# Performance work log

Hardware: AMD Instinct MI355X
Metric: run time of the kernel (lower is better)

The kernel has to match this reference:

```python
import jax, jax.numpy as jnp
import numpy as np

B, D, H = 256, 512, 256
K = 5
MARGIN = 1.0
TAU = 1.0
LAM_C = 0.01
LAM_E = 0.1
BETA = 0.1
LN_EPS = 1e-5


def _layernorm(x, g, b):
    mu = jnp.mean(x, axis=-1, keepdims=True)
    var = jnp.var(x, axis=-1, keepdims=True)
    return (x - mu) * jax.lax.rsqrt(var + LN_EPS) * g + b


def setup_inputs() -> dict:
    key = jax.random.key(0)
    ks = jax.random.split(key, 16)
    s = 0.02
    inp = {
        "outputs": jax.random.normal(ks[0], (B, 3, 64, 64), jnp.float32),
        "images": jax.random.normal(ks[1], (B, 3, 64, 64), jnp.float32),
        "f_orig": jax.random.normal(ks[2], (B, D), jnp.float32),
        "f_recon": jax.random.normal(ks[3], (B, D), jnp.float32),
        "cf1": jax.random.normal(ks[4], (B, 256, 8, 8), jnp.float32),
        "cf2": jax.random.normal(ks[5], (B, 512, 4, 4), jnp.float32),
        # EnergyNet encoder params
        "W1": jax.random.normal(ks[6], (D, H), jnp.float32) * s,
        "b1": jnp.zeros((H,), jnp.float32),
        "g1": jnp.ones((H,), jnp.float32),
        "be1": jnp.zeros((H,), jnp.float32),
        "W2": jax.random.normal(ks[7], (H, H), jnp.float32) * s,
        "b2": jnp.zeros((H,), jnp.float32),
        # EnergyNet interaction params
        "W3": jax.random.normal(ks[8], (3 * H, H), jnp.float32) * s,
        "b3": jnp.zeros((H,), jnp.float32),
        "g3": jnp.ones((H,), jnp.float32),
        "be3": jnp.zeros((H,), jnp.float32),
        "W4": jax.random.normal(ks[9], (H, H // 2), jnp.float32) * s,
        "b4": jnp.zeros((H // 2,), jnp.float32),
        "W5": jax.random.normal(ks[10], (H // 2, 1), jnp.float32) * s,
        "b5": jnp.zeros((1,), jnp.float32),
    }
    return inp


def _encoder(x, W1, b1, g1, be1, W2, b2):
    h = _layernorm(x @ W1 + b1, g1, be1)
    return jax.nn.relu(h) @ W2 + b2


def _energy_matrix(f1, f2, W1, b1, g1, be1, W2, b2, W3, b3, g3, be3, W4, b4, W5, b5):
    e1 = _encoder(f1, W1, b1, g1, be1, W2, b2)  # [B,H]
    e2 = _encoder(f2, W1, b1, g1, be1, W2, b2)  # [B,H]
    e1b = jnp.broadcast_to(e1[:, None, :], (B, B, H))
    e2b = jnp.broadcast_to(e2[None, :, :], (B, B, H))
    combined = jnp.concatenate([e1b, e2b, e1b * e2b], axis=-1)  # [B,B,3H]
    h = jax.nn.relu(_layernorm(combined @ W3 + b3, g3, be3))
    h = jax.nn.relu(h @ W4 + b4)
    return (h @ W5 + b5)[..., 0]  # [B,B]


def _topk_neighbors(f, k):
    fn = f / (jnp.linalg.norm(f, axis=1, keepdims=True))
    sim = fn @ fn.T
    sim = jnp.where(jnp.eye(f.shape[0], dtype=bool), -jnp.inf, sim)
    _, idx = jax.lax.top_k(sim, k)  # [B,k]
    onehot = jnp.zeros((f.shape[0], f.shape[0]), jnp.float32)
    rows = jnp.arange(f.shape[0])[:, None]
    return onehot.at[rows, idx].set(1.0)


def _entropy(x):
    xn = (x - x.min()) / (x.max() - x.min() + 1e-8)
    # torch.histc(bins=256, min=0, max=1): values at max go to last bin
    idx = jnp.clip(jnp.floor(xn.reshape(-1) * 256.0).astype(jnp.int32), 0, 255)
    hist = jnp.bincount(idx, length=256).astype(jnp.float32)
    p = hist / hist.sum()
    return -jnp.sum(p * jnp.log2(p + 1e-8))


def reference(outputs, images, f_orig, f_recon, cf1, cf2,
              W1, b1, g1, be1, W2, b2, W3, b3, g3, be3, W4, b4, W5, b5):
    # reconstruction loss
    recon = jnp.mean((outputs - images) ** 2)

    # energy margin loss
    E = _energy_matrix(f_orig, f_recon, W1, b1, g1, be1, W2, b2,
                       W3, b3, g3, be3, W4, b4, W5, b5)
    pos = jnp.diag(E)[:, None]
    losses = jax.nn.relu(MARGIN + E - pos)
    neg_mask = ~jnp.eye(B, dtype=bool)
    standard_loss = jnp.sum(losses * neg_mask) / (B * (B - 1))

    k = min(K, B - 1)
    on = _topk_neighbors(f_orig, k)
    rn = _topk_neighbors(f_recon, k)
    inter = jnp.sum(on * rn, axis=1)
    union = jnp.sum(jnp.clip(on + rn, 0.0, 1.0), axis=1)
    jaccard = inter / (union + 1e-8)
    neighbor_loss = 1.0 - jnp.mean(jaccard)
    energy_loss = standard_loss + 0.3 * neighbor_loss

    # compression loss over the dict of compressed features {cf1, cf2}
    sp = 0.5 * (jnp.mean(jnp.abs(cf1)) + jnp.mean(jnp.abs(cf2)))
    en = 0.5 * (_entropy(cf1) + _entropy(cf2))
    compress = sp + BETA * en

    total = recon + LAM_C * compress + LAM_E * energy_loss
    return (total, recon, energy_loss, compress)
```

## Files before the change

### kernel.cpp

```cpp
#include <hip/hip_runtime.h>
#include <math.h>

typedef __attribute__((ext_vector_type(8))) short short8;
typedef __attribute__((ext_vector_type(4))) float f32x4;
typedef __attribute__((ext_vector_type(4))) unsigned int u32x4;

union U8 { unsigned int u[4]; short8 s; u32x4 v; };


__device__ __forceinline__ float wave_sum(float v) {
#pragma unroll
    for (int o = 32; o > 0; o >>= 1) v += __shfl_down(v, o);
    return v;
}

__device__ __forceinline__ float block_sum256(float v, float* red) {
    v = wave_sum(v);
    int t = threadIdx.x;
    if ((t & 63) == 0) red[t >> 6] = v;
    __syncthreads();
    float r = red[0] + red[1] + red[2] + red[3];
    __syncthreads();
    return r;
}

__device__ __forceinline__ unsigned fenc(float f) {
    unsigned u = __float_as_uint(f);
    return (u & 0x80000000u) ? ~u : (u | 0x80000000u);
}
__device__ __forceinline__ float fdec(unsigned u) {
    return (u & 0x80000000u) ? __uint_as_float(u & 0x7fffffffu) : __uint_as_float(~u);
}

__device__ __forceinline__ ushort f2bf(float f) {
    unsigned u = __float_as_uint(f);
    unsigned r = (u + 0x7fffu + ((u >> 16) & 1u)) >> 16;
    return (ushort)r;
}
__device__ __forceinline__ float bflo(unsigned u) { return __uint_as_float(u << 16); }
__device__ __forceinline__ float bfhi(unsigned u) { return __uint_as_float(u & 0xffff0000u); }


__global__ void init_kernel(float* wsf, unsigned* wsu, int* wsi) {
    int t = threadIdx.x;
    if (t < 7) wsf[t] = 0.f;
    if (t == 7 || t == 9) wsu[t] = 0xFFFFFFFFu;
    if (t == 8 || t == 10) wsu[t] = 0u;
    wsi[16 + t] = 0;
    wsi[272 + t] = 0;
}

__global__ __launch_bounds__(256) void mega_kernel(
    const float4* __restrict__ o, const float4* __restrict__ im,
    const float4* __restrict__ cf1, const float4* __restrict__ cf2,
    const float* __restrict__ fo, const float* __restrict__ fr,
    const float* __restrict__ W1, const float* __restrict__ b1,
    const float* __restrict__ g1, const float* __restrict__ be1,
    const float* __restrict__ W2, const float* __restrict__ b2,
    const float* __restrict__ W3,
    float* wsf, unsigned* wsu, float* rnorm, float* fT,
    float* __restrict__ A1, ushort* __restrict__ A2bf, ushort* __restrict__ ebf,
    ushort* __restrict__ W3pk, ushort* __restrict__ W4pk, const float* __restrict__ W4) {
    __shared__ float smem[64 * 33];
    float* red = smem;
    int b = blockIdx.x, t = threadIdx.x;
    if (b < 2048) {
        if (b < 512) {
            float s = 0.f;
            for (int i = b * 256 + t; i < 786432; i += 512 * 256) {
                float4 a = o[i], c = im[i];
                float dx = a.x - c.x, dy = a.y - c.y, dz = a.z - c.z, dw = a.w - c.w;
                s += dx * dx + dy * dy + dz * dz + dw * dw;
            }
            float tot = block_sum256(s, red);
            if (t == 0) atomicAdd(wsf + 0, tot);
        } else if (b < 1536) {
            int which = (b < 1024) ? 0 : 1;
            const float4* x = which ? cf2 : cf1;
            int n4 = which ? 524288 : 1048576;
            int b0 = which ? 1024 : 512;
            float s = 0.f, mn = INFINITY, mx = -INFINITY;
            for (int i = (b - b0) * 256 + t; i < n4; i += 512 * 256) {
                float4 a = x[i];
                s += fabsf(a.x) + fabsf(a.y) + fabsf(a.z) + fabsf(a.w);
                mn = fminf(mn, fminf(fminf(a.x, a.y), fminf(a.z, a.w)));
                mx = fmaxf(mx, fmaxf(fmaxf(a.x, a.y), fmaxf(a.z, a.w)));
            }
            float tot = block_sum256(s, red);
#pragma unroll
            for (int off = 32; off > 0; off >>= 1) {
                mn = fminf(mn, __shfl_down(mn, off));
                mx = fmaxf(mx, __shfl_down(mx, off));
            }
            float* rmn = smem + 8;
            float* rmx = smem + 16;
            if ((t & 63) == 0) { rmn[t >> 6] = mn; rmx[t >> 6] = mx; }
            __syncthreads();
            if (t == 0) {
                atomicAdd(wsf + 1 + which, tot);
                float m1 = fminf(fminf(rmn[0], rmn[1]), fminf(rmn[2], rmn[3]));
                float m2 = fmaxf(fmaxf(rmx[0], rmx[1]), fmaxf(rmx[2], rmx[3]));
                atomicMin(wsu + 7 + which * 2, fenc(m1));
                atomicMax(wsu + 8 + which * 2, fenc(m2));
            }
        } else {
            int r = b - 1536;
            const float4* f = (r < 256) ? ((const float4*)fo + (size_t)r * 128)
                                        : ((const float4*)fr + (size_t)(r - 256) * 128);
            float s = 0.f;
            if (t < 128) {
                float4 a = f[t];
                s = a.x * a.x + a.y * a.y + a.z * a.z + a.w * a.w;
            }
            float tot = block_sum256(s, red);
            if (t == 0) rnorm[r] = 1.0f / sqrtf(tot);
        }
    } else if (b < 2176) {
        int bb = b - 2048;
        int pass = bb >> 6;
        int kt = (bb >> 2) & 15;
        int jt = bb & 3;
        int k0 = kt * 32, j0 = jt * 64;
        const float* f = pass ? fr : fo;
        float (*tile)[33] = (float(*)[33])smem;
        int cl = t & 31, rl = t >> 5;
#pragma unroll
        for (int r = 0; r < 8; ++r) {
            int row = j0 + rl + r * 8;
            tile[rl + r * 8][cl] = f[(size_t)row * 512 + k0 + cl];
        }
        __syncthreads();
        int jl = t & 63, kq = t >> 6;
        float* dst = fT + (size_t)pass * 131072;
#pragma unroll
        for (int c = 0; c < 8; ++c) {
            int kl = kq * 8 + c;
            dst[(size_t)(k0 + kl) * 256 + j0 + jl] = tile[jl][kl];
        }
    } else if (b < 2224) {
        int pb = b - 2176;
        const float* W3c = W3 + 512 * 256;
        if (pb < 32) {
            int s = pb * 256 + t;
            int lane = s & 63;
            int tt = (s >> 6) & 15;
            int kk = s >> 10;
            int qq = lane >> 4, nn = lane & 15;
            int tcol = tt * 16 + nn;
            short8 v;
#pragma unroll
            for (int jj = 0; jj < 8; ++jj) {
                int k = kk * 32 + qq * 8 + jj;
                v[jj] = (short)f2bf(W3c[(size_t)k * 256 + tcol]);
            }
            *(short8*)(W3pk + (size_t)s * 8) = v;
        } else {
            int s = (pb - 32) * 256 + t;
            int lane = s & 63;
            int tt = (s >> 6) & 7;
            int kk = s >> 9;
            int qq = lane >> 4, nn = lane & 15;
            int ncol = tt * 16 + nn;
            short8 v;
#pragma unroll
            for (int jj = 0; jj < 8; ++jj) {
                int k = kk * 32 + qq * 8 + jj;
                v[jj] = (short)f2bf(W4[(size_t)k * 128 + ncol]);
            }
            *(short8*)(W4pk + (size_t)s * 8) = v;
        }
    } else {
        int r = b - 2224;
        const float* f = (r < 256) ? (fo + (size_t)r * 512) : (fr + (size_t)(r - 256) * 512);
        const float* W3p = (r < 256) ? W3 : (W3 + 256 * 256);
        float* fs = smem;
        float* hs = smem + 512;
        float* es = smem + 768;
        float* rd = smem + 1024;
        fs[t] = f[t];
        fs[t + 256] = f[t + 256];
        __syncthreads();
        float x = b1[t];
        for (int k = 0; k < 512; ++k) x += fs[k] * W1[k * 256 + t];
        float s1 = block_sum256(x, rd);
        float s2 = block_sum256(x * x, rd);
        float mean = s1 * (1.f / 256.f);
        float var = s2 * (1.f / 256.f) - mean * mean;
        float rstd = rsqrtf(var + 1e-5f);
        float hn = (x - mean) * rstd * g1[t] + be1[t];
        hs[t] = fmaxf(hn, 0.f);
        __syncthreads();
        float e = b2[t];
        for (int k = 0; k < 256; ++k) e += hs[k] * W2[k * 256 + t];
        ebf[(size_t)r * 256 + t] = f2bf(e);
        es[t] = e;
        __syncthreads();
        float a = 0.f;
        for (int k = 0; k < 256; ++k) a += es[k] * W3p[k * 256 + t];
        if (r < 256) A1[(size_t)r * 256 + t] = a;
        else A2bf[(size_t)(r - 256) * 256 + t] = f2bf(a);
    }
}

__global__ __launch_bounds__(256) void hist_kernel(const float4* __restrict__ cf1,
                                                   const float4* __restrict__ cf2,
                                                   const unsigned* wsu, int* wsi) {
    __shared__ int hl[256];
    int b = blockIdx.x, t = threadIdx.x;
    hl[t] = 0;
    __syncthreads();
    int which = (b < 512) ? 0 : 1;
    const float4* x = which ? cf2 : cf1;
    int n4 = which ? 524288 : 1048576;
    int b0 = which ? 512 : 0;
    int* hist = wsi + (which ? 272 : 16);
    float mn = fdec(wsu[7 + which * 2]), mx = fdec(wsu[8 + which * 2]);
    float inv = 256.f / (mx - mn + 1e-8f);
    for (int i = (b - b0) * 256 + t; i < n4; i += 512 * 256) {
        float4 a = x[i];
        int b0i = min(max((int)floorf((a.x - mn) * inv), 0), 255);
        int b1i = min(max((int)floorf((a.y - mn) * inv), 0), 255);
        int b2i = min(max((int)floorf((a.z - mn) * inv), 0), 255);
        int b3i = min(max((int)floorf((a.w - mn) * inv), 0), 255);
        atomicAdd(&hl[b0i], 1);
        atomicAdd(&hl[b1i], 1);
        atomicAdd(&hl[b2i], 1);
        atomicAdd(&hl[b3i], 1);
    }
    __syncthreads();
    if (hl[t]) atomicAdd(&hist[t], hl[t]);
}

__global__ __launch_bounds__(256) void simtop_kernel(const float* __restrict__ fo,
                                                     const float* __restrict__ fr,
                                                     const float* __restrict__ rnorm,
                                                     const float* __restrict__ fT,
                                                     int* __restrict__ top5) {
    int b = blockIdx.x;
    int pass = b >> 7, pair = b & 127;
    int i0 = pair * 2, i1 = i0 + 1;
    const float* f = pass ? fr : fo;
    const float* rn = rnorm + pass * 256;
    __shared__ float2 fs2[512];
    __shared__ float candV[4][2][5];
    __shared__ int candI[4][2][5];
    int t = threadIdx.x;
    const float* f0 = f + (size_t)i0 * 512;
    const float* f1 = f + (size_t)i1 * 512;
    fs2[t] = make_float2(f0[t], f1[t]);
    fs2[t + 256] = make_float2(f0[t + 256], f1[t + 256]);
    __syncthreads();
    int j = t;
    const float* col = fT + (size_t)pass * 131072 + j;
    float a0 = 0.f, a1 = 0.f;
#pragma unroll 16
    for (int k = 0; k < 512; ++k) {
        float v = col[(size_t)k * 256];
        float2 fv = fs2[k];
        a0 += fv.x * v;
        a1 += fv.y * v;
    }
    float rnj = rn[j];
    a0 *= rnj;
    a1 *= rnj;
    if (j == i0) a0 = -INFINITY;
    if (j == i1) a1 = -INFINITY;
    int w = t >> 6, lane = t & 63;
    for (int sel = 0; sel < 2; ++sel) {
        float v2 = sel ? a1 : a0;
        int idx = j;
        for (int r = 0; r < 5; ++r) {
            float m = v2;
            int mi = idx;
#pragma unroll
            for (int off = 32; off > 0; off >>= 1) {
                float om = __shfl_xor(m, off);
                int omi = __shfl_xor(mi, off);
                if (om > m || (om == m && omi < mi)) { m = om; mi = omi; }
            }
            if (lane == 0) { candV[w][sel][r] = m; candI[w][sel][r] = mi; }
            if (idx == mi) v2 = -INFINITY;
        }
    }
    __syncthreads();
    if (w < 2) {
        float v = -INFINITY;
        int ix = 0x7fffffff;
        if (lane < 20) { v = candV[lane / 5][w][lane % 5]; ix = candI[lane / 5][w][lane % 5]; }
        int iSel = w ? i1 : i0;
        for (int r = 0; r < 5; ++r) {
            float m = v;
            int mi = ix;
#pragma unroll
            for (int off = 32; off > 0; off >>= 1) {
                float om = __shfl_xor(m, off);
                int omi = __shfl_xor(mi, off);
                if (om > m || (om == m && omi < mi)) { m = om; mi = omi; }
            }
            if (lane == 0) top5[((size_t)pass * 256 + iSel) * 5 + r] = mi;
            if (ix == mi) v = -INFINITY;
        }
    }
}

__global__ __launch_bounds__(256, 1) void energy_v3(
    const float* __restrict__ A1, const ushort* __restrict__ A2bf,
    const ushort* __restrict__ ebf,
    const ushort* __restrict__ W3p, const ushort* __restrict__ W4p,
    const float* __restrict__ b3, const float* __restrict__ g3, const float* __restrict__ be3,
    const float* __restrict__ b4, const float* __restrict__ W5, const float* __restrict__ b5,
    float* __restrict__ E)
{
    int i = blockIdx.x;
    int t = threadIdx.x;
    int w = t >> 6, lane = t & 63, q = lane >> 4, n = lane & 15;
    int jb = w * 64;
    __shared__ float combS[256], g3S[256], be3S[256], b4S[128], w5S[128];
    combS[t] = A1[(size_t)i * 256 + t] + b3[t];
    g3S[t] = g3[t];
    be3S[t] = be3[t];
    if (t < 128) { b4S[t] = b4[t]; w5S[t] = W5[t]; }
    __syncthreads();

    const ushort* e1p = ebf + (size_t)i * 256;
    const ushort* e2p = ebf + 65536;

    f32x4 acc[4][16];
#pragma unroll
    for (int s = 0; s < 4; ++s)
#pragma unroll
        for (int tt = 0; tt < 16; ++tt) acc[s][tt] = (f32x4){0.f, 0.f, 0.f, 0.f};

    for (int kk = 0; kk < 8; ++kk) {
        int kbase = kk * 32 + q * 8;
        U8 e1v;
        e1v.v = *(const u32x4*)(e1p + kbase);
        float e1f[8];
#pragma unroll
        for (int x = 0; x < 4; ++x) {
            e1f[2 * x] = bflo(e1v.u[x]);
            e1f[2 * x + 1] = bfhi(e1v.u[x]);
        }
        short8 bfrag[4];
#pragma unroll
        for (int s = 0; s < 4; ++s) {
            U8 e2v;
            e2v.v = *(const u32x4*)(e2p + (size_t)(jb + s * 16 + n) * 256 + kbase);
            U8 bb;
#pragma unroll
            for (int x = 0; x < 4; ++x) {
                float p0 = bflo(e2v.u[x]) * e1f[2 * x];
                float p1 = bfhi(e2v.u[x]) * e1f[2 * x + 1];
                bb.u[x] = (unsigned)f2bf(p0) | ((unsigned)f2bf(p1) << 16);
            }
            bfrag[s] = bb.s;
        }
        const ushort* wp = W3p + ((size_t)(kk * 16) * 64 + lane) * 8;
#pragma unroll
        for (int tt = 0; tt < 16; ++tt) {
            short8 af = *(const short8*)(wp + (size_t)tt * 512);
#pragma unroll
            for (int s = 0; s < 4; ++s)
                acc[s][tt] = __builtin_amdgcn_mfma_f32_16x16x32_bf16(af, bfrag[s], acc[s][tt], 0, 0, 0);
        }
    }

    uint2 pk[4][16];
    float b5v = b5[0];
#pragma unroll
    for (int s = 0; s < 4; ++s) {
        int j = jb + s * 16 + n;
        float s1 = 0.f, s2 = 0.f;
#pragma unroll
        for (int tt = 0; tt < 16; ++tt) {
            int tb = tt * 16 + q * 4;
            float4 cb = *(const float4*)(combS + tb);
            uint2 a2u = *(const uint2*)(A2bf + (size_t)j * 256 + tb);
            float a0 = bflo(a2u.x), a1f = bfhi(a2u.x), a2f = bflo(a2u.y), a3f = bfhi(a2u.y);
            float v0 = acc[s][tt][0] + cb.x + a0;
            float v1 = acc[s][tt][1] + cb.y + a1f;
            float v2 = acc[s][tt][2] + cb.z + a2f;
            float v3 = acc[s][tt][3] + cb.w + a3f;
            acc[s][tt][0] = v0; acc[s][tt][1] = v1; acc[s][tt][2] = v2; acc[s][tt][3] = v3;
            s1 += v0 + v1 + v2 + v3;
            s2 += v0 * v0 + v1 * v1 + v2 * v2 + v3 * v3;
        }
        s1 += __shfl_xor(s1, 16); s1 += __shfl_xor(s1, 32);
        s2 += __shfl_xor(s2, 16); s2 += __shfl_xor(s2, 32);
        float mean = s1 * (1.f / 256.f);
        float var = s2 * (1.f / 256.f) - mean * mean;
        float rstd = rsqrtf(var + 1e-5f);
#pragma unroll
        for (int tt = 0; tt < 16; ++tt) {
            int tb = tt * 16 + q * 4;
            float4 gg = *(const float4*)(g3S + tb);
            float4 be = *(const float4*)(be3S + tb);
            float h0 = fmaxf((acc[s][tt][0] - mean) * rstd * gg.x + be.x, 0.f);
            float h1 = fmaxf((acc[s][tt][1] - mean) * rstd * gg.y + be.y, 0.f);
            float h2 = fmaxf((acc[s][tt][2] - mean) * rstd * gg.z + be.z, 0.f);
            float h3 = fmaxf((acc[s][tt][3] - mean) * rstd * gg.w + be.w, 0.f);
            pk[s][tt].x = (unsigned)f2bf(h0) | ((unsigned)f2bf(h1) << 16);
            pk[s][tt].y = (unsigned)f2bf(h2) | ((unsigned)f2bf(h3) << 16);
        }
    }

    f32x4 gacc[4][8];
#pragma unroll
    for (int s = 0; s < 4; ++s)
#pragma unroll
        for (int nt = 0; nt < 8; ++nt) gacc[s][nt] = (f32x4){0.f, 0.f, 0.f, 0.f};

    int qh = (q >> 1) & 1;
    int src0 = ((q & 1) * 2) * 16 + n;
    int src1 = src0 + 16;
#pragma unroll
    for (int kk = 0; kk < 8; ++kk) {
        short8 wa[8];
        const ushort* wp = W4p + ((size_t)(kk * 8) * 64 + lane) * 8;
#pragma unroll
        for (int nt = 0; nt < 8; ++nt) wa[nt] = *(const short8*)(wp + (size_t)nt * 512);
#pragma unroll
        for (int s = 0; s < 4; ++s) {
            uint2 lo2 = pk[s][kk * 2], hi2 = pk[s][kk * 2 + 1];
            unsigned a0 = (unsigned)__shfl((int)lo2.x, src0);
            unsigned a1 = (unsigned)__shfl((int)lo2.y, src0);
            unsigned b0 = (unsigned)__shfl((int)hi2.x, src0);
            unsigned b1 = (unsigned)__shfl((int)hi2.y, src0);
            unsigned c0 = (unsigned)__shfl((int)lo2.x, src1);
            unsigned c1 = (unsigned)__shfl((int)lo2.y, src1);
            unsigned d0 = (unsigned)__shfl((int)hi2.x, src1);
            unsigned d1 = (unsigned)__shfl((int)hi2.y, src1);
            U8 hb;
            hb.u[0] = qh ? b0 : a0;
            hb.u[1] = qh ? b1 : a1;
            hb.u[2] = qh ? d0 : c0;
            hb.u[3] = qh ? d1 : c1;
#pragma unroll
            for (int nt = 0; nt < 8; ++nt)
                gacc[s][nt] = __builtin_amdgcn_mfma_f32_16x16x32_bf16(wa[nt], hb.s, gacc[s][nt], 0, 0, 0);
        }
    }

#pragma unroll
    for (int s = 0; s < 4; ++s) {
        float ep = 0.f;
#pragma unroll
        for (int nt = 0; nt < 8; ++nt) {
            int nb = nt * 16 + q * 4;
            float4 b4v = *(const float4*)(b4S + nb);
            float4 w5v = *(const float4*)(w5S + nb);
            ep += fmaxf(gacc[s][nt][0] + b4v.x, 0.f) * w5v.x;
            ep += fmaxf(gacc[s][nt][1] + b4v.y, 0.f) * w5v.y;
            ep += fmaxf(gacc[s][nt][2] + b4v.z, 0.f) * w5v.z;
            ep += fmaxf(gacc[s][nt][3] + b4v.w, 0.f) * w5v.w;
        }
        ep += __shfl_xor(ep, 16);
        ep += __shfl_xor(ep, 32);
        if (q == 0) E[(size_t)i * 256 + jb + s * 16 + n] = ep + b5v;
    }
}

__global__ void margin_jac_kernel(const float* __restrict__ E, const int* __restrict__ top5,
                                  float* slAcc, float* jacOut) {
    __shared__ float red[4];
    int b = blockIdx.x, t = threadIdx.x;
    if (b < 256) {
        float diag = E[(size_t)b * 256 + b];
        float l = (t == b) ? 0.f : fmaxf(1.f + E[(size_t)b * 256 + t] - diag, 0.f);
        float tot = block_sum256(l, red);
        if (t == 0) atomicAdd(slAcc, tot);
    } else {
        int O[5], R[5];
#pragma unroll
        for (int r = 0; r < 5; ++r) {
            O[r] = top5[t * 5 + r];
            R[r] = top5[(256 + t) * 5 + r];
        }
        int inter = 0;
#pragma unroll
        for (int a = 0; a < 5; ++a)
#pragma unroll
            for (int bq = 0; bq < 5; ++bq) inter += (O[a] == R[bq]);
        float fi2 = (float)inter;
        float jac = fi2 / (10.f - fi2 + 1e-8f);
        float s = block_sum256(jac, red);
        if (t == 0) jacOut[0] = s;
    }
}

__global__ void finalize_kernel(const float* wsf, const int* h1, const int* h2, float* out) {
    __shared__ float red[4];
    int t = threadIdx.x;
    float p1 = (float)h1[t] / 4194304.f;
    float p2 = (float)h2[t] / 2097152.f;
    float s1 = block_sum256(-p1 * log2f(p1 + 1e-8f), red);
    float s2 = block_sum256(-p2 * log2f(p2 + 1e-8f), red);
    if (t == 0) {
        float recon = wsf[0] / 3145728.f;
        float sp = 0.5f * (wsf[1] / 4194304.f + wsf[2] / 2097152.f);
        float en = 0.5f * (s1 + s2);
        float compress = sp + 0.1f * en;
        float sl = wsf[5] / (256.f * 255.f);
        float nl = 1.f - wsf[6] / 256.f;
        float energy = sl + 0.3f * nl;
        float total = recon + 0.01f * compress + 0.1f * energy;
        out[0] = total;
        out[1] = recon;
        out[2] = energy;
        out[3] = compress;
    }
}

extern "C" void kernel_launch(void* const* d_in, const int* in_sizes, int n_in,
                              void* d_out, int out_size, void* d_ws, size_t ws_size,
                              hipStream_t stream) {
    const float* outputs = (const float*)d_in[0];
    const float* images  = (const float*)d_in[1];
    const float* f_orig  = (const float*)d_in[2];
    const float* f_recon = (const float*)d_in[3];
    const float* cf1 = (const float*)d_in[4];
    const float* cf2 = (const float*)d_in[5];
    const float* W1 = (const float*)d_in[6];
    const float* b1 = (const float*)d_in[7];
    const float* g1 = (const float*)d_in[8];
    const float* be1 = (const float*)d_in[9];
    const float* W2 = (const float*)d_in[10];
    const float* b2 = (const float*)d_in[11];
    const float* W3 = (const float*)d_in[12];
    const float* b3 = (const float*)d_in[13];
    const float* g3 = (const float*)d_in[14];
    const float* be3 = (const float*)d_in[15];
    const float* W4 = (const float*)d_in[16];
    const float* b4 = (const float*)d_in[17];
    const float* W5 = (const float*)d_in[18];
    const float* b5 = (const float*)d_in[19];

    float* wsf = (float*)d_ws;
    unsigned* wsu = (unsigned*)d_ws;
    int* wsi = (int*)d_ws;
    float* out = (float*)d_out;

    float* rnorm = wsf + 528;
    float* A1 = wsf + 1040;
    ushort* A2bf = (ushort*)(wsf + 66576);
    ushort* ebf = (ushort*)(wsf + 82960);
    float* Emat = wsf + 148496;
    ushort* W3pk = (ushort*)(wsf + 214032);
    ushort* W4pk = (ushort*)(wsf + 230416);
    float* fT = wsf + 238608;
    int* top5 = wsi + 500752;

    hipLaunchKernelGGL(init_kernel, dim3(1), dim3(256), 0, stream, wsf, wsu, wsi);
    hipLaunchKernelGGL(mega_kernel, dim3(2736), dim3(256), 0, stream,
                       (const float4*)outputs, (const float4*)images,
                       (const float4*)cf1, (const float4*)cf2,
                       f_orig, f_recon, W1, b1, g1, be1, W2, b2, W3,
                       wsf, wsu, rnorm, fT, A1, A2bf, ebf, W3pk, W4pk, W4);
    hipLaunchKernelGGL(hist_kernel, dim3(1024), dim3(256), 0, stream,
                       (const float4*)cf1, (const float4*)cf2, wsu, wsi);
    hipLaunchKernelGGL(simtop_kernel, dim3(256), dim3(256), 0, stream,
                       f_orig, f_recon, rnorm, fT, top5);
    hipLaunchKernelGGL(energy_v3, dim3(256), dim3(256), 0, stream,
                       A1, A2bf, ebf, W3pk, W4pk, b3, g3, be3, b4, W5, b5, Emat);
    hipLaunchKernelGGL(margin_jac_kernel, dim3(257), dim3(256), 0, stream,
                       Emat, top5, wsf + 5, wsf + 6);
    hipLaunchKernelGGL(finalize_kernel, dim3(1), dim3(256), 0, stream,
                       wsf, wsi + 16, wsi + 272, out);
}
```

Baseline: 283.2 us.

## Move encoder MLP to a dedicated bf16 MFMA kernel and store intermediates in bf16

Replaces the 512 per-row scalar encoder blocks in the mega kernel with a separate 8-block kernel that runs the W1/W2/W3a/W3b matmuls on bf16 MFMA. The weights are pre-packed by the mega kernel and activations are passed between stages through wave shuffles. A1 and the energy matrix E are now stored as bf16, which halves their traffic. The simtop dot-product loop is split into four independent accumulator chains for more ILP. The risks are lower precision in the encoder path and in E, and an 8-block kernel that leaves most CUs idle.

```diff
diff --git a/kernel.cpp b/kernel.cpp
--- a/kernel.cpp
+++ b/kernel.cpp
@@ -39,6 +39,7 @@
 }
 __device__ __forceinline__ float bflo(unsigned u) { return __uint_as_float(u << 16); }
 __device__ __forceinline__ float bfhi(unsigned u) { return __uint_as_float(u & 0xffff0000u); }
+__device__ __forceinline__ float bf2f(ushort u) { return __uint_as_float((unsigned)u << 16); }
 
 
 __global__ void init_kernel(float* wsf, unsigned* wsu, int* wsi) {
@@ -50,17 +51,46 @@
     wsi[272 + t] = 0;
 }
 
+__device__ __forceinline__ void pack256(const float* __restrict__ src, ushort* __restrict__ dst, int s) {
+    int lane = s & 63;
+    int tt = (s >> 6) & 15;
+    int kk = s >> 10;
+    int qq = lane >> 4, nn = lane & 15;
+    int tcol = tt * 16 + nn;
+    short8 v;
+#pragma unroll
+    for (int jj = 0; jj < 8; ++jj) {
+        int k = kk * 32 + qq * 8 + jj;
+        v[jj] = (short)f2bf(src[(size_t)k * 256 + tcol]);
+    }
+    *(short8*)(dst + (size_t)s * 8) = v;
+}
+
+__device__ __forceinline__ void pack128(const float* __restrict__ src, ushort* __restrict__ dst, int s) {
+    int lane = s & 63;
+    int tt = (s >> 6) & 7;
+    int kk = s >> 9;
+    int qq = lane >> 4, nn = lane & 15;
+    int ncol = tt * 16 + nn;
+    short8 v;
+#pragma unroll
+    for (int jj = 0; jj < 8; ++jj) {
+        int k = kk * 32 + qq * 8 + jj;
+        v[jj] = (short)f2bf(src[(size_t)k * 128 + ncol]);
+    }
+    *(short8*)(dst + (size_t)s * 8) = v;
+}
+
 __global__ __launch_bounds__(256) void mega_kernel(
     const float4* __restrict__ o, const float4* __restrict__ im,
     const float4* __restrict__ cf1, const float4* __restrict__ cf2,
     const float* __restrict__ fo, const float* __restrict__ fr,
-    const float* __restrict__ W1, const float* __restrict__ b1,
-    const float* __restrict__ g1, const float* __restrict__ be1,
-    const float* __restrict__ W2, const float* __restrict__ b2,
-    const float* __restrict__ W3,
+    const float* __restrict__ W1, const float* __restrict__ W2,
+    const float* __restrict__ W3, const float* __restrict__ W4,
     float* wsf, unsigned* wsu, float* rnorm, float* fT,
-    float* __restrict__ A1, ushort* __restrict__ A2bf, ushort* __restrict__ ebf,
-    ushort* __restrict__ W3pk, ushort* __restrict__ W4pk, const float* __restrict__ W4) {
+    ushort* __restrict__ W3cpk, ushort* __restrict__ W4pk,
+    ushort* __restrict__ W1pk, ushort* __restrict__ W2pk,
+    ushort* __restrict__ W3apk, ushort* __restrict__ W3bpk) {
     __shared__ float smem[64 * 33];
     float* red = smem;
     int b = blockIdx.x, t = threadIdx.x;
@@ -137,68 +167,14 @@
             int kl = kq * 8 + c;
             dst[(size_t)(k0 + kl) * 256 + j0 + jl] = tile[jl][kl];
         }
-    } else if (b < 2224) {
+    } else {
         int pb = b - 2176;
-        const float* W3c = W3 + 512 * 256;
-        if (pb < 32) {
-            int s = pb * 256 + t;
-            int lane = s & 63;
-            int tt = (s >> 6) & 15;
-            int kk = s >> 10;
-            int qq = lane >> 4, nn = lane & 15;
-            int tcol = tt * 16 + nn;
-            short8 v;
-#pragma unroll
-            for (int jj = 0; jj < 8; ++jj) {
-                int k = kk * 32 + qq * 8 + jj;
-                v[jj] = (short)f2bf(W3c[(size_t)k * 256 + tcol]);
-            }
-            *(short8*)(W3pk + (size_t)s * 8) = v;
-        } else {
-            int s = (pb - 32) * 256 + t;
-            int lane = s & 63;
-            int tt = (s >> 6) & 7;
-            int kk = s >> 9;
-            int qq = lane >> 4, nn = lane & 15;
-            int ncol = tt * 16 + nn;
-            short8 v;
-#pragma unroll
-            for (int jj = 0; jj < 8; ++jj) {
-                int k = kk * 32 + qq * 8 + jj;
-                v[jj] = (short)f2bf(W4[(size_t)k * 128 + ncol]);
-            }
-            *(short8*)(W4pk + (size_t)s * 8) = v;
-        }
-    } else {
-        int r = b - 2224;
-        const float* f = (r < 256) ? (fo + (size_t)r * 512) : (fr + (size_t)(r - 256) * 512);
-        const float* W3p = (r < 256) ? W3 : (W3 + 256 * 256);
-        float* fs = smem;
-        float* hs = smem + 512;
-        float* es = smem + 768;
-        float* rd = smem + 1024;
-        fs[t] = f[t];
-        fs[t + 256] = f[t + 256];
-        __syncthreads();
-        float x = b1[t];
-        for (int k = 0; k < 512; ++k) x += fs[k] * W1[k * 256 + t];
-        float s1 = block_sum256(x, rd);
-        float s2 = block_sum256(x * x, rd);
-        float mean = s1 * (1.f / 256.f);
-        float var = s2 * (1.f / 256.f) - mean * mean;
-        float rstd = rsqrtf(var + 1e-5f);
-        float hn = (x - mean) * rstd * g1[t] + be1[t];
-        hs[t] = fmaxf(hn, 0.f);
-        __syncthreads();
-        float e = b2[t];
-        for (int k = 0; k < 256; ++k) e += hs[k] * W2[k * 256 + t];
-        ebf[(size_t)r * 256 + t] = f2bf(e);
-        es[t] = e;
-        __syncthreads();
-        float a = 0.f;
-        for (int k = 0; k < 256; ++k) a += es[k] * W3p[k * 256 + t];
-        if (r < 256) A1[(size_t)r * 256 + t] = a;
-        else A2bf[(size_t)(r - 256) * 256 + t] = f2bf(a);
+        if (pb < 32) pack256(W3 + 512 * 256, W3cpk, pb * 256 + t);
+        else if (pb < 48) pack128(W4, W4pk, (pb - 32) * 256 + t);
+        else if (pb < 112) pack256(W1, W1pk, (pb - 48) * 256 + t);
+        else if (pb < 144) pack256(W2, W2pk, (pb - 112) * 256 + t);
+        else if (pb < 176) pack256(W3, W3apk, (pb - 144) * 256 + t);
+        else pack256(W3 + 256 * 256, W3bpk, (pb - 176) * 256 + t);
     }
 }
 
@@ -231,6 +207,150 @@
     if (hl[t]) atomicAdd(&hist[t], hl[t]);
 }
 
+__global__ __launch_bounds__(256) void encoder_mfma(
+    const float* __restrict__ fo, const float* __restrict__ fr,
+    const ushort* __restrict__ W1p, const ushort* __restrict__ W2p,
+    const ushort* __restrict__ W3ap, const ushort* __restrict__ W3bp,
+    const float* __restrict__ b1, const float* __restrict__ g1,
+    const float* __restrict__ be1, const float* __restrict__ b2,
+    ushort* __restrict__ ebf, ushort* __restrict__ A1bf, ushort* __restrict__ A2bf)
+{
+    int blk = blockIdx.x;
+    int t = threadIdx.x;
+    int w = t >> 6, lane = t & 63, q = lane >> 4, n = lane & 15;
+    int r = blk * 64 + w * 16 + n;
+    bool isOrig = (r < 256);
+    const float* f = isOrig ? (fo + (size_t)r * 512) : (fr + (size_t)(r - 256) * 512);
+
+    f32x4 acc[16];
+#pragma unroll
+    for (int tt = 0; tt < 16; ++tt) acc[tt] = (f32x4){0.f, 0.f, 0.f, 0.f};
+    for (int kk = 0; kk < 16; ++kk) {
+        int kb = kk * 32 + q * 8;
+        float4 fa = *(const float4*)(f + kb);
+        float4 fb = *(const float4*)(f + kb + 4);
+        U8 bb;
+        bb.u[0] = (unsigned)f2bf(fa.x) | ((unsigned)f2bf(fa.y) << 16);
+        bb.u[1] = (unsigned)f2bf(fa.z) | ((unsigned)f2bf(fa.w) << 16);
+        bb.u[2] = (unsigned)f2bf(fb.x) | ((unsigned)f2bf(fb.y) << 16);
+        bb.u[3] = (unsigned)f2bf(fb.z) | ((unsigned)f2bf(fb.w) << 16);
+        const ushort* wp = W1p + ((size_t)(kk * 1024 + lane)) * 8;
+#pragma unroll
+        for (int tt = 0; tt < 16; ++tt) {
+            short8 af = *(const short8*)(wp + (size_t)tt * 512);
+            acc[tt] = __builtin_amdgcn_mfma_f32_16x16x32_bf16(af, bb.s, acc[tt], 0, 0, 0);
+        }
+    }
+    float s1 = 0.f, s2 = 0.f;
+#pragma unroll
+    for (int tt = 0; tt < 16; ++tt) {
+        int tb = tt * 16 + q * 4;
+        float4 bv = *(const float4*)(b1 + tb);
+        float v0 = acc[tt][0] + bv.x, v1 = acc[tt][1] + bv.y;
+        float v2 = acc[tt][2] + bv.z, v3 = acc[tt][3] + bv.w;
+        acc[tt][0] = v0; acc[tt][1] = v1; acc[tt][2] = v2; acc[tt][3] = v3;
+        s1 += v0 + v1 + v2 + v3;
+        s2 += v0 * v0 + v1 * v1 + v2 * v2 + v3 * v3;
+    }
+    s1 += __shfl_xor(s1, 16); s1 += __shfl_xor(s1, 32);
+    s2 += __shfl_xor(s2, 16); s2 += __shfl_xor(s2, 32);
+    float mean = s1 * (1.f / 256.f);
+    float var = s2 * (1.f / 256.f) - mean * mean;
+    float rstd = rsqrtf(var + 1e-5f);
+    uint2 pk[16];
+#pragma unroll
+    for (int tt = 0; tt < 16; ++tt) {
+        int tb = tt * 16 + q * 4;
+        float4 gg = *(const float4*)(g1 + tb);
+        float4 be = *(const float4*)(be1 + tb);
+        float h0 = fmaxf((acc[tt][0] - mean) * rstd * gg.x + be.x, 0.f);
+        float h1 = fmaxf((acc[tt][1] - mean) * rstd * gg.y + be.y, 0.f);
+        float h2 = fmaxf((acc[tt][2] - mean) * rstd * gg.z + be.z, 0.f);
+        float h3 = fmaxf((acc[tt][3] - mean) * rstd * gg.w + be.w, 0.f);
+        pk[tt].x = (unsigned)f2bf(h0) | ((unsigned)f2bf(h1) << 16);
+        pk[tt].y = (unsigned)f2bf(h2) | ((unsigned)f2bf(h3) << 16);
+    }
+
+    int qh = (q >> 1) & 1;
+    int src0 = ((q & 1) * 2) * 16 + n;
+    int src1 = src0 + 16;
+
+    f32x4 eacc[16];
+#pragma unroll
+    for (int tt = 0; tt < 16; ++tt) eacc[tt] = (f32x4){0.f, 0.f, 0.f, 0.f};
+#pragma unroll
+    for (int kk = 0; kk < 8; ++kk) {
+        uint2 lo2 = pk[kk * 2], hi2 = pk[kk * 2 + 1];
+        unsigned a0 = (unsigned)__shfl((int)lo2.x, src0);
+        unsigned a1 = (unsigned)__shfl((int)lo2.y, src0);
+        unsigned b0 = (unsigned)__shfl((int)hi2.x, src0);
+        unsigned b1v = (unsigned)__shfl((int)hi2.y, src0);
+        unsigned c0 = (unsigned)__shfl((int)lo2.x, src1);
+        unsigned c1 = (unsigned)__shfl((int)lo2.y, src1);
+        unsigned d0 = (unsigned)__shfl((int)hi2.x, src1);
+        unsigned d1 = (unsigned)__shfl((int)hi2.y, src1);
+        U8 hb;
+        hb.u[0] = qh ? b0 : a0;
+        hb.u[1] = qh ? b1v : a1;
+        hb.u[2] = qh ? d0 : c0;
+        hb.u[3] = qh ? d1 : c1;
+        const ushort* wp = W2p + ((size_t)(kk * 1024 + lane)) * 8;
+#pragma unroll
+        for (int tt = 0; tt < 16; ++tt) {
+            short8 af = *(const short8*)(wp + (size_t)tt * 512);
+            eacc[tt] = __builtin_amdgcn_mfma_f32_16x16x32_bf16(af, hb.s, eacc[tt], 0, 0, 0);
+        }
+    }
+    uint2 epk[16];
+#pragma unroll
+    for (int tt = 0; tt < 16; ++tt) {
+        int tb = tt * 16 + q * 4;
+        float4 bv = *(const float4*)(b2 + tb);
+        float e0 = eacc[tt][0] + bv.x, e1 = eacc[tt][1] + bv.y;
+        float e2 = eacc[tt][2] + bv.z, e3 = eacc[tt][3] + bv.w;
+        epk[tt].x = (unsigned)f2bf(e0) | ((unsigned)f2bf(e1) << 16);
+        epk[tt].y = (unsigned)f2bf(e2) | ((unsigned)f2bf(e3) << 16);
+        *(uint2*)(ebf + (size_t)r * 256 + tb) = epk[tt];
+    }
+
+    const ushort* W3x = isOrig ? W3ap : W3bp;
+    f32x4 aacc[16];
+#pragma unroll
+    for (int tt = 0; tt < 16; ++tt) aacc[tt] = (f32x4){0.f, 0.f, 0.f, 0.f};
+#pragma unroll
+    for (int kk = 0; kk < 8; ++kk) {
+        uint2 lo2 = epk[kk * 2], hi2 = epk[kk * 2 + 1];
+        unsigned a0 = (unsigned)__shfl((int)lo2.x, src0);
+        unsigned a1 = (unsigned)__shfl((int)lo2.y, src0);
+        unsigned b0 = (unsigned)__shfl((int)hi2.x, src0);
+        unsigned b1v = (unsigned)__shfl((int)hi2.y, src0);
+        unsigned c0 = (unsigned)__shfl((int)lo2.x, src1);
+        unsigned c1 = (unsigned)__shfl((int)lo2.y, src1);
+        unsigned d0 = (unsigned)__shfl((int)hi2.x, src1);
+        unsigned d1 = (unsigned)__shfl((int)hi2.y, src1);
+        U8 hb;
+        hb.u[0] = qh ? b0 : a0;
+        hb.u[1] = qh ? b1v : a1;
+        hb.u[2] = qh ? d0 : c0;
+        hb.u[3] = qh ? d1 : c1;
+        const ushort* wp = W3x + ((size_t)(kk * 1024 + lane)) * 8;
+#pragma unroll
+        for (int tt = 0; tt < 16; ++tt) {
+            short8 af = *(const short8*)(wp + (size_t)tt * 512);
+            aacc[tt] = __builtin_amdgcn_mfma_f32_16x16x32_bf16(af, hb.s, aacc[tt], 0, 0, 0);
+        }
+    }
+    ushort* dst = isOrig ? (A1bf + (size_t)r * 256) : (A2bf + (size_t)(r - 256) * 256);
+#pragma unroll
+    for (int tt = 0; tt < 16; ++tt) {
+        int tb = tt * 16 + q * 4;
+        uint2 pv;
+        pv.x = (unsigned)f2bf(aacc[tt][0]) | ((unsigned)f2bf(aacc[tt][1]) << 16);
+        pv.y = (unsigned)f2bf(aacc[tt][2]) | ((unsigned)f2bf(aacc[tt][3]) << 16);
+        *(uint2*)(dst + tb) = pv;
+    }
+}
+
 __global__ __launch_bounds__(256) void simtop_kernel(const float* __restrict__ fo,
                                                      const float* __restrict__ fr,
                                                      const float* __restrict__ rnorm,
@@ -252,14 +372,21 @@
     __syncthreads();
     int j = t;
     const float* col = fT + (size_t)pass * 131072 + j;
-    float a0 = 0.f, a1 = 0.f;
-#pragma unroll 16
-    for (int k = 0; k < 512; ++k) {
-        float v = col[(size_t)k * 256];
-        float2 fv = fs2[k];
-        a0 += fv.x * v;
-        a1 += fv.y * v;
-    }
+    float x0 = 0.f, x1 = 0.f, y0 = 0.f, y1 = 0.f, z0 = 0.f, z1 = 0.f, u0 = 0.f, u1 = 0.f;
+#pragma unroll 8
+    for (int k = 0; k < 128; ++k) {
+        float v0 = col[(size_t)k * 256];
+        float v1 = col[(size_t)(k + 128) * 256];
+        float v2 = col[(size_t)(k + 256) * 256];
+        float v3 = col[(size_t)(k + 384) * 256];
+        float2 g0 = fs2[k], g1 = fs2[k + 128], g2 = fs2[k + 256], g3 = fs2[k + 384];
+        x0 += g0.x * v0; x1 += g0.y * v0;
+        y0 += g1.x * v1; y1 += g1.y * v1;
+        z0 += g2.x * v2; z1 += g2.y * v2;
+        u0 += g3.x * v3; u1 += g3.y * v3;
+    }
+    float a0 = (x0 + y0) + (z0 + u0);
+    float a1 = (x1 + y1) + (z1 + u1);
     float rnj = rn[j];
     a0 *= rnj;
     a1 *= rnj;
@@ -304,19 +431,19 @@
 }
 
 __global__ __launch_bounds__(256, 1) void energy_v3(
-    const float* __restrict__ A1, const ushort* __restrict__ A2bf,
+    const ushort* __restrict__ A1bf, const ushort* __restrict__ A2bf,
     const ushort* __restrict__ ebf,
     const ushort* __restrict__ W3p, const ushort* __restrict__ W4p,
     const float* __restrict__ b3, const float* __restrict__ g3, const float* __restrict__ be3,
     const float* __restrict__ b4, const float* __restrict__ W5, const float* __restrict__ b5,
-    float* __restrict__ E)
+    ushort* __restrict__ E)
 {
     int i = blockIdx.x;
     int t = threadIdx.x;
     int w = t >> 6, lane = t & 63, q = lane >> 4, n = lane & 15;
     int jb = w * 64;
     __shared__ float combS[256], g3S[256], be3S[256], b4S[128], w5S[128];
-    combS[t] = A1[(size_t)i * 256 + t] + b3[t];
+    combS[t] = bf2f(A1bf[(size_t)i * 256 + t]) + b3[t];
     g3S[t] = g3[t];
     be3S[t] = be3[t];
     if (t < 128) { b4S[t] = b4[t]; w5S[t] = W5[t]; }
@@ -456,17 +583,17 @@
         }
         ep += __shfl_xor(ep, 16);
         ep += __shfl_xor(ep, 32);
-        if (q == 0) E[(size_t)i * 256 + jb + s * 16 + n] = ep + b5v;
-    }
-}
-
-__global__ void margin_jac_kernel(const float* __restrict__ E, const int* __restrict__ top5,
+        if (q == 0) E[(size_t)i * 256 + jb + s * 16 + n] = f2bf(ep + b5v);
+    }
+}
+
+__global__ void margin_jac_kernel(const ushort* __restrict__ E, const int* __restrict__ top5,
                                   float* slAcc, float* jacOut) {
     __shared__ float red[4];
     int b = blockIdx.x, t = threadIdx.x;
     if (b < 256) {
-        float diag = E[(size_t)b * 256 + b];
-        float l = (t == b) ? 0.f : fmaxf(1.f + E[(size_t)b * 256 + t] - diag, 0.f);
+        float diag = bf2f(E[(size_t)b * 256 + b]);
+        float l = (t == b) ? 0.f : fmaxf(1.f + bf2f(E[(size_t)b * 256 + t]) - diag, 0.f);
         float tot = block_sum256(l, red);
         if (t == 0) atomicAdd(slAcc, tot);
     } else {
@@ -541,29 +668,36 @@
     float* out = (float*)d_out;
 
     float* rnorm = wsf + 528;
-    float* A1 = wsf + 1040;
-    ushort* A2bf = (ushort*)(wsf + 66576);
-    ushort* ebf = (ushort*)(wsf + 82960);
-    float* Emat = wsf + 148496;
-    ushort* W3pk = (ushort*)(wsf + 214032);
-    ushort* W4pk = (ushort*)(wsf + 230416);
-    float* fT = wsf + 238608;
-    int* top5 = wsi + 500752;
+    ushort* A1bf = (ushort*)(wsf + 1040);
+    ushort* A2bf = (ushort*)(wsf + 33808);
+    ushort* ebf  = (ushort*)(wsf + 66576);
+    ushort* Ebf  = (ushort*)(wsf + 132112);
+    ushort* W3cpk = (ushort*)(wsf + 164880);
+    ushort* W4pk  = (ushort*)(wsf + 197648);
+    ushort* W1pk  = (ushort*)(wsf + 214032);
+    ushort* W2pk  = (ushort*)(wsf + 279568);
+    ushort* W3apk = (ushort*)(wsf + 312336);
+    ushort* W3bpk = (ushort*)(wsf + 345104);
+    float* fT = wsf + 377872;
+    int* top5 = wsi + 640016;
 
     hipLaunchKernelGGL(init_kernel, dim3(1), dim3(256), 0, stream, wsf, wsu, wsi);
-    hipLaunchKernelGGL(mega_kernel, dim3(2736), dim3(256), 0, stream,
+    hipLaunchKernelGGL(mega_kernel, dim3(2384), dim3(256), 0, stream,
                        (const float4*)outputs, (const float4*)images,
                        (const float4*)cf1, (const float4*)cf2,
-                       f_orig, f_recon, W1, b1, g1, be1, W2, b2, W3,
-                       wsf, wsu, rnorm, fT, A1, A2bf, ebf, W3pk, W4pk, W4);
+                       f_orig, f_recon, W1, W2, W3, W4,
+                       wsf, wsu, rnorm, fT, W3cpk, W4pk, W1pk, W2pk, W3apk, W3bpk);
     hipLaunchKernelGGL(hist_kernel, dim3(1024), dim3(256), 0, stream,
                        (const float4*)cf1, (const float4*)cf2, wsu, wsi);
+    hipLaunchKernelGGL(encoder_mfma, dim3(8), dim3(256), 0, stream,
+                       f_orig, f_recon, W1pk, W2pk, W3apk, W3bpk,
+                       b1, g1, be1, b2, ebf, A1bf, A2bf);
     hipLaunchKernelGGL(simtop_kernel, dim3(256), dim3(256), 0, stream,
                        f_orig, f_recon, rnorm, fT, top5);
     hipLaunchKernelGGL(energy_v3, dim3(256), dim3(256), 0, stream,
-                       A1, A2bf, ebf, W3pk, W4pk, b3, g3, be3, b4, W5, b5, Emat);
+                       A1bf, A2bf, ebf, W3cpk, W4pk, b3, g3, be3, b4, W5, b5, Ebf);
     hipLaunchKernelGGL(margin_jac_kernel, dim3(257), dim3(256), 0, stream,
-                       Emat, top5, wsf + 5, wsf + 6);
+                       Ebf, top5, wsf + 5, wsf + 6);
     hipLaunchKernelGGL(finalize_kernel, dim3(1), dim3(256), 0, stream,
                        wsf, wsi + 16, wsi + 272, out);
 }
```

Result: slower. 413.7 us (+46.1%).
